# Optimization experiments

Measured on AMD Instinct MI355X. Metric: run time of the kernel, lower is better.

Reference implementation:

```python
import jax, jax.numpy as jnp
import numpy as np

N, M, D = 4096, 50000, 512


def setup_inputs() -> dict:
    key = jax.random.key(0)
    k1, k2, k3, k4, k5 = jax.random.split(key, 5)
    return {
        "X_trans": jax.random.normal(k1, (N, D), dtype=jnp.float32),
        "Y_tgt": jax.random.normal(k2, (N, D), dtype=jnp.float32),
        "Z_src": jax.random.normal(k3, (M, D), dtype=jnp.float32),
        "Z_tgt": jax.random.normal(k4, (M, D), dtype=jnp.float32),
        "back_emb": jax.random.normal(k5, (N, D), dtype=jnp.float32),
        "knn": 10,
    }


def _l2norm(x):
    # row-wise L2 normalize, matching x / x.norm(2,1,keepdim=True)
    return x / jnp.linalg.norm(x, axis=1, keepdims=True)


def _getknn(sc, k):
    # torch: topk(10) values gathered then sliced to first k, summed / k
    vals = jax.lax.top_k(sc, 10)[0]  # [rows, 10], sorted descending
    return vals[:, :k].sum() / k


def reference(X_trans, Y_tgt, Z_src, Z_tgt, back_emb, knn):
    src_emb = _l2norm(X_trans)
    tgt_emb = _l2norm(Y_tgt)
    zs = _l2norm(Z_src)
    zt = _l2norm(Z_tgt)
    bk = _l2norm(back_emb)
    f = 2.0 * jnp.sum(src_emb * tgt_emb)
    fk0 = _getknn(src_emb @ zt.T, knn)   # [N, M] scores src->tgt vocab
    fk1 = _getknn(bk @ zs.T, knn)        # [N, M] scores back->src vocab
    f = f - fk0 - fk1
    return -f / X_trans.shape[0]
```

## Files before the change

kernel.cpp:

```cpp
#include <hip/hip_runtime.h>
#include <hip/hip_bf16.h>
#include <stdint.h>

#define N_ROWS 4096
#define DIM 512
#define M_COLS 50000
#define GTOT (M_COLS/16)
#define SPLITS 16
#define TOPK 10

typedef __attribute__((ext_vector_type(8))) short bf16x8;
typedef __attribute__((ext_vector_type(4))) float f32x4;
typedef __attribute__((address_space(1))) const uint32_t gu32;
typedef __attribute__((address_space(3))) uint32_t lu32;

__device__ __forceinline__ float waveSum(float v){
  #pragma unroll
  for (int off=32; off>0; off>>=1) v += __shfl_xor(v, off, 64);
  return v;
}

__device__ __forceinline__ unsigned short f2bf(float x){
  __hip_bfloat16 h = __float2bfloat16(x);
  return *reinterpret_cast<unsigned short*>(&h);
}

__global__ __launch_bounds__(128) void norm_bf16_kernel(const float* __restrict__ in,
                                                        unsigned short* __restrict__ out){
  const int row = blockIdx.x;
  const int t = threadIdx.x;
  const float4 v = *reinterpret_cast<const float4*>(in + (size_t)row*DIM + t*4);
  float ss = v.x*v.x + v.y*v.y + v.z*v.z + v.w*v.w;
  ss = waveSum(ss);
  __shared__ float sred[2];
  if ((t & 63) == 0) sred[t>>6] = ss;
  __syncthreads();
  const float r = rsqrtf(sred[0] + sred[1]);
  ushort4 o;
  o.x = f2bf(v.x*r); o.y = f2bf(v.y*r); o.z = f2bf(v.z*r); o.w = f2bf(v.w*r);
  *reinterpret_cast<ushort4*>(out + (size_t)row*DIM + t*4) = o;
}

__global__ __launch_bounds__(128) void dotS_kernel(const float* __restrict__ X, const float* __restrict__ Y,
                                                   unsigned short* __restrict__ srcb, float* __restrict__ S_acc){
  const int row = blockIdx.x;
  const int t = threadIdx.x;
  const float4 x = *reinterpret_cast<const float4*>(X + (size_t)row*DIM + t*4);
  const float4 y = *reinterpret_cast<const float4*>(Y + (size_t)row*DIM + t*4);
  float ssx = x.x*x.x+x.y*x.y+x.z*x.z+x.w*x.w;
  float ssy = y.x*y.x+y.y*y.y+y.z*y.z+y.w*y.w;
  float sxy = x.x*y.x+x.y*y.y+x.z*y.z+x.w*y.w;
  ssx = waveSum(ssx); ssy = waveSum(ssy); sxy = waveSum(sxy);
  __shared__ float r0[2], r1[2], r2[2];
  if ((t&63)==0){ r0[t>>6]=ssx; r1[t>>6]=ssy; r2[t>>6]=sxy; }
  __syncthreads();
  const float tx = r0[0]+r0[1], ty = r1[0]+r1[1], txy = r2[0]+r2[1];
  const float rx = rsqrtf(tx);
  ushort4 o; o.x=f2bf(x.x*rx); o.y=f2bf(x.y*rx); o.z=f2bf(x.z*rx); o.w=f2bf(x.w*rx);
  *reinterpret_cast<ushort4*>(srcb + (size_t)row*DIM + t*4) = o;
  if (t == 0) atomicAdd(S_acc, txy * rsqrtf(tx*ty));
}

__global__ __launch_bounds__(256, 2) void mm_topk_kernel(const unsigned short* __restrict__ A,
                                                         const unsigned short* __restrict__ Z,
                                                         float* __restrict__ topk){
  __shared__ __align__(16) unsigned short tiles[2][16*DIM];
  const int l = threadIdx.x & 63;
  const int w = threadIdx.x >> 6;
  const int rb = blockIdx.x;
  const int sp = blockIdx.y;
  const int gps = (GTOT + SPLITS - 1)/SPLITS;
  const int g0 = sp*gps;
  const int g1 = min(GTOT, g0 + gps);

  bf16x8 a0[16], a1[16];
  {
    const unsigned short* ap = A + (size_t)(rb*128 + w*32 + (l&15))*DIM + ((l>>4)*8);
    #pragma unroll
    for (int t=0; t<16; ++t){
      a0[t] = *reinterpret_cast<const bf16x8*>(ap + 32*t);
      a1[t] = *reinterpret_cast<const bf16x8*>(ap + 16*DIM + 32*t);
    }
  }

  float lst[2][4], thr[2][4];
  #pragma unroll
  for (int s=0;s<2;++s)
    #pragma unroll
    for (int j=0;j<4;++j){ lst[s][j] = -__builtin_inff(); thr[s][j] = -__builtin_inff(); }

  auto stage = [&](int g, int b){
    const int c0 = g*16;
    #pragma unroll
    for (int q=0; q<4; ++q){
      const int i = w*4 + q;
      const unsigned short* src = Z + (size_t)(c0 + (l&15))*DIM + i*32 + (l>>4)*8;
      unsigned short* dst = &tiles[b][i*DIM];
      __builtin_amdgcn_global_load_lds((gu32*)src, (lu32*)dst, 16, 0, 0);
    }
  };

  auto topk_update = [&](f32x4& acc, float* ls, float* th){
    #pragma unroll
    for (int j=0;j<4;++j){
      bool myc = acc[j] > th[j];
      unsigned long long m = __ballot(myc);
      while (m){
        const unsigned long long grp = (m >> (l & 48)) & 0xFFFFull;
        if (grp){
          const int src = (l & 48) + __builtin_ctzll(grp);
          const float v = __shfl(acc[j], src, 64);
          float nxt = __shfl(ls[j], (l==63)?63:(l+1), 64);
          if ((l & 15) >= 9) nxt = __builtin_inff();
          ls[j] = fminf(nxt, fmaxf(ls[j], v));
          th[j] = __shfl(ls[j], l & 48, 64);
          if (l == src) myc = false;
        }
        m = __ballot(myc);
      }
    }
  };

  stage(g0, 0);
  for (int g=g0; g<g1; ++g){
    const int buf = (g - g0) & 1;
    __syncthreads();
    if (g+1 < g1) stage(g+1, buf^1);
    f32x4 acc0 = {0.f,0.f,0.f,0.f};
    f32x4 acc1 = {0.f,0.f,0.f,0.f};
    const unsigned short* tb = tiles[buf];
    #pragma unroll
    for (int t=0;t<16;++t){
      bf16x8 b = *reinterpret_cast<const bf16x8*>(tb + t*DIM + l*8);
      acc0 = __builtin_amdgcn_mfma_f32_16x16x32_bf16(a0[t], b, acc0, 0, 0, 0);
      acc1 = __builtin_amdgcn_mfma_f32_16x16x32_bf16(a1[t], b, acc1, 0, 0, 0);
    }
    topk_update(acc0, lst[0], thr[0]);
    topk_update(acc1, lst[1], thr[1]);
  }

  if ((l & 15) < TOPK){
    #pragma unroll
    for (int s=0;s<2;++s)
      #pragma unroll
      for (int j=0;j<4;++j){
        const int row = rb*128 + w*32 + s*16 + (l>>4)*4 + j;
        topk[((size_t)row*SPLITS + sp)*TOPK + (l & 15)] = lst[s][j];
      }
  }
}

__global__ __launch_bounds__(256) void merge_kernel(const float* __restrict__ tk, const int* __restrict__ knnp,
                                                    float* __restrict__ FK){
  const int n = blockIdx.x*256 + threadIdx.x;
  float ls[TOPK];
  #pragma unroll
  for (int i=0;i<TOPK;++i) ls[i] = -__builtin_inff();
  const float* p = tk + (size_t)n*(SPLITS*TOPK);
  for (int i=0;i<SPLITS*TOPK;++i){
    const float v = p[i];
    if (v > ls[0]){
      ls[0] = v;
      #pragma unroll
      for (int k=0;k<TOPK-1;++k){
        if (ls[k] > ls[k+1]){ float tmp=ls[k]; ls[k]=ls[k+1]; ls[k+1]=tmp; }
      }
    }
  }
  const int kk = min(max(knnp[0],1),TOPK);
  float s = 0.f;
  #pragma unroll
  for (int i=0;i<TOPK;++i) if (i < kk) s += ls[TOPK-1-i];
  s = waveSum(s);
  __shared__ float red[4];
  if ((threadIdx.x & 63)==0) red[threadIdx.x>>6] = s;
  __syncthreads();
  if (threadIdx.x==0) atomicAdd(FK, red[0]+red[1]+red[2]+red[3]);
}

__global__ void finalize_kernel(const float* __restrict__ S_acc, const float* __restrict__ FK,
                                const int* __restrict__ knnp, float* __restrict__ out){
  const float k = (float)max(knnp[0],1);
  out[0] = (FK[0]/k - 2.0f*S_acc[0]) / (float)N_ROWS;
}

extern "C" void kernel_launch(void* const* d_in, const int* in_sizes, int n_in,
                              void* d_out, int out_size, void* d_ws, size_t ws_size,
                              hipStream_t stream){
  const float* X  = (const float*)d_in[0];
  const float* Y  = (const float*)d_in[1];
  const float* Zs = (const float*)d_in[2];
  const float* Zt = (const float*)d_in[3];
  const float* Bk = (const float*)d_in[4];
  const int* knn  = (const int*)d_in[5];

  char* ws = (char*)d_ws;
  float* S_acc = (float*)ws;
  float* FK    = (float*)(ws + 4);
  float* topk0 = (float*)(ws + 64);
  float* topk1 = topk0 + (size_t)N_ROWS*SPLITS*TOPK;
  unsigned short* srcb = (unsigned short*)(ws + 64 + 2*(size_t)N_ROWS*SPLITS*TOPK*4);
  unsigned short* bkb  = srcb + (size_t)N_ROWS*DIM;
  unsigned short* Zb   = bkb  + (size_t)N_ROWS*DIM;

  hipMemsetAsync(d_ws, 0, 64, stream);
  dotS_kernel<<<N_ROWS, 128, 0, stream>>>(X, Y, srcb, S_acc);
  norm_bf16_kernel<<<N_ROWS, 128, 0, stream>>>(Bk, bkb);
  norm_bf16_kernel<<<M_COLS, 128, 0, stream>>>(Zt, Zb);
  mm_topk_kernel<<<dim3(N_ROWS/128, SPLITS), 256, 0, stream>>>(srcb, Zb, topk0);
  norm_bf16_kernel<<<M_COLS, 128, 0, stream>>>(Zs, Zb);
  mm_topk_kernel<<<dim3(N_ROWS/128, SPLITS), 256, 0, stream>>>(bkb, Zb, topk1);
  merge_kernel<<<(2*N_ROWS)/256, 256, 0, stream>>>(topk0, knn, FK);
  finalize_kernel<<<1, 1, 0, stream>>>(S_acc, FK, knn, (float*)d_out);
}
```

Baseline: 1.089 ms.

## Load Z tiles directly into registers with rolling prefetch instead of LDS staging

```diff
diff --git a/kernel.cpp b/kernel.cpp
--- a/kernel.cpp
+++ b/kernel.cpp
@@ -11,8 +11,6 @@
 
 typedef __attribute__((ext_vector_type(8))) short bf16x8;
 typedef __attribute__((ext_vector_type(4))) float f32x4;
-typedef __attribute__((address_space(1))) const uint32_t gu32;
-typedef __attribute__((address_space(3))) uint32_t lu32;
 
 __device__ __forceinline__ float waveSum(float v){
   #pragma unroll
@@ -61,10 +59,9 @@
   if (t == 0) atomicAdd(S_acc, txy * rsqrtf(tx*ty));
 }
 
-__global__ __launch_bounds__(256, 2) void mm_topk_kernel(const unsigned short* __restrict__ A,
-                                                         const unsigned short* __restrict__ Z,
-                                                         float* __restrict__ topk){
-  __shared__ __align__(16) unsigned short tiles[2][16*DIM];
+__global__ __launch_bounds__(256) void mm_topk_kernel(const unsigned short* __restrict__ A,
+                                                      const unsigned short* __restrict__ Z,
+                                                      float* __restrict__ topk){
   const int l = threadIdx.x & 63;
   const int w = threadIdx.x >> 6;
   const int rb = blockIdx.x;
@@ -83,22 +80,16 @@
     }
   }
 
+  const unsigned short* zb = Z + (size_t)(l&15)*DIM + ((l>>4)*8);
+  auto LD = [&](int g, int t){
+    return *reinterpret_cast<const bf16x8*>(zb + (size_t)g*(16*DIM) + t*32);
+  };
+
   float lst[2][4], thr[2][4];
   #pragma unroll
   for (int s=0;s<2;++s)
     #pragma unroll
     for (int j=0;j<4;++j){ lst[s][j] = -__builtin_inff(); thr[s][j] = -__builtin_inff(); }
-
-  auto stage = [&](int g, int b){
-    const int c0 = g*16;
-    #pragma unroll
-    for (int q=0; q<4; ++q){
-      const int i = w*4 + q;
-      const unsigned short* src = Z + (size_t)(c0 + (l&15))*DIM + i*32 + (l>>4)*8;
-      unsigned short* dst = &tiles[b][i*DIM];
-      __builtin_amdgcn_global_load_lds((gu32*)src, (lu32*)dst, 16, 0, 0);
-    }
-  };
 
   auto topk_update = [&](f32x4& acc, float* ls, float* th){
     #pragma unroll
@@ -121,22 +112,24 @@
     }
   };
 
-  stage(g0, 0);
+  bf16x8 b[8];
+  #pragma unroll
+  for (int t=0;t<8;++t) b[t] = LD(g0, t);
+
   for (int g=g0; g<g1; ++g){
-    const int buf = (g - g0) & 1;
-    __syncthreads();
-    if (g+1 < g1) stage(g+1, buf^1);
+    const int gn = (g+1 < g1) ? g+1 : g0;
     f32x4 acc0 = {0.f,0.f,0.f,0.f};
     f32x4 acc1 = {0.f,0.f,0.f,0.f};
-    const unsigned short* tb = tiles[buf];
     #pragma unroll
     for (int t=0;t<16;++t){
-      bf16x8 b = *reinterpret_cast<const bf16x8*>(tb + t*DIM + l*8);
-      acc0 = __builtin_amdgcn_mfma_f32_16x16x32_bf16(a0[t], b, acc0, 0, 0, 0);
-      acc1 = __builtin_amdgcn_mfma_f32_16x16x32_bf16(a1[t], b, acc1, 0, 0, 0);
+      bf16x8 cur = b[t & 7];
+      b[t & 7] = (t < 8) ? LD(g, t+8) : LD(gn, t-8);
+      acc0 = __builtin_amdgcn_mfma_f32_16x16x32_bf16(a0[t], cur, acc0, 0, 0, 0);
+      acc1 = __builtin_amdgcn_mfma_f32_16x16x32_bf16(a1[t], cur, acc1, 0, 0, 0);
     }
     topk_update(acc0, lst[0], thr[0]);
     topk_update(acc1, lst[1], thr[1]);
+    __builtin_amdgcn_s_barrier();
   }
 
   if ((l & 15) < TOPK){
```

New measurement: 1.878 ms. 1.72x slower.
